# Performance work log

Hardware: AMD Instinct MI355X
Metric: run time of the kernel (lower is better)

Reference implementation:

```python
import jax, jax.numpy as jnp
import numpy as np

WINDOW_SIZE = 2
SOFTMAX_TEMP = 0.01
EPS = 1e-12  # F.normalize default eps


def _l2_normalize(x, axis):
    n = jnp.sqrt(jnp.sum(x * x, axis=axis, keepdims=True))
    return x / jnp.maximum(n, EPS)


def setup_inputs() -> dict:
    key = jax.random.key(0)
    k1, k2, k3 = jax.random.split(key, 3)
    B, C, N = 16, 128, 4096
    return {
        "keypoint_coords": jax.random.normal(k1, (B, 2, N), dtype=jnp.float32),
        "keypoint_weights": jax.random.uniform(k2, (B, 1, N), dtype=jnp.float32),
        "keypoint_desc": jax.random.normal(k3, (B, C, N), dtype=jnp.float32),
    }


def reference(keypoint_coords, keypoint_weights, keypoint_desc):
    # split interleaved src/tgt frames along batch
    src_coords = keypoint_coords[::WINDOW_SIZE]    # [b,2,N]
    tgt_coords = keypoint_coords[1::WINDOW_SIZE]   # [b,2,M]
    src_weights = keypoint_weights[::WINDOW_SIZE]  # [b,1,N]
    tgt_weights = keypoint_weights[1::WINDOW_SIZE] # [b,1,M]
    src_desc = keypoint_desc[::WINDOW_SIZE]        # [b,C,N]
    tgt_desc = keypoint_desc[1::WINDOW_SIZE]       # [b,C,M]

    C = src_desc.shape[1]
    src_desc_norm = _l2_normalize(src_desc, axis=1)
    tgt_desc_norm = _l2_normalize(tgt_desc, axis=1)

    # cosine similarity matrix [b,N,M]
    match_vals = jnp.einsum("bcn,bcm->bnm", src_desc_norm, tgt_desc_norm)
    soft_match_vals = jax.nn.softmax(match_vals / SOFTMAX_TEMP, axis=2)

    # reuse the attention matrix for three value matmuls
    pseudo_coords = jnp.einsum("bcm,bnm->bcn", tgt_coords, soft_match_vals)   # [b,2,N]
    pseudo_desc = jnp.einsum("bcm,bnm->bcn", tgt_desc, soft_match_vals)       # [b,C,N]
    pseudo_desc = _l2_normalize(pseudo_desc, axis=1)
    pseudo_weights = jnp.einsum("bim,bnm->bin", tgt_weights, soft_match_vals) # [b,1,N]

    desc_match_score = jnp.sum(src_desc * pseudo_desc, axis=1, keepdims=True) / float(C)
    match_weights = 0.5 * (desc_match_score + 1.0) * src_weights * pseudo_weights
    return pseudo_coords, match_weights
```

## Files before the change

kernel.cpp:

```cpp
#include <hip/hip_runtime.h>
#include <math.h>

#define C 128
#define N 4096
#define BP 8
#define TN 64

typedef __attribute__((ext_vector_type(8))) short bf16x8;
typedef __attribute__((ext_vector_type(16))) float f32x16;
typedef __attribute__((ext_vector_type(4))) int i32x4;
typedef __attribute__((ext_vector_type(16))) int i32x16;

#define PREP_OFF 65536
#define FRAGS_PER_MT 18
#define BLOB_BYTES ((size_t)BP * 128 * FRAGS_PER_MT * 1024)

__device__ __forceinline__ unsigned short bf16rnd(float x) {
  unsigned u = __float_as_uint(x);
  u += 0x7fffu + ((u >> 16) & 1u);
  return (unsigned short)(u >> 16);
}
__device__ __forceinline__ float bf16up(unsigned short h) {
  return __uint_as_float(((unsigned)h) << 16);
}
__device__ __forceinline__ int rne2(float x, float y) {
  unsigned ux = __float_as_uint(x); ux += 0x7fffu + ((ux >> 16) & 1u);
  unsigned uy = __float_as_uint(y); uy += 0x7fffu + ((uy >> 16) & 1u);
  return (int)__builtin_amdgcn_perm(uy, ux, 0x07060302u);
}
__device__ __forceinline__ int trunc2(float x, float y) {
  return (int)__builtin_amdgcn_perm(__float_as_uint(y), __float_as_uint(x), 0x07060302u);
}
__device__ __forceinline__ float truncres(float x) {
  return x - __uint_as_float(__float_as_uint(x) & 0xffff0000u);
}
__device__ __forceinline__ int pk4(int a, int b, int c, int d) {
  return (a & 255) | ((b & 255) << 8) | ((c & 255) << 16) | ((d & 255) << 24);
}

__global__ __launch_bounds__(256) void knorm_inv(const float* __restrict__ desc,
                                                 float* __restrict__ inv) {
  int n = blockIdx.x * 256 + threadIdx.x;
  int b = 2 * blockIdx.y + 1;
  const float* d = desc + (size_t)b * C * N + n;
  float ssq = 0.f;
#pragma unroll 8
  for (int c = 0; c < C; ++c) {
    float v = d[(size_t)c * N];
    ssq = fmaf(v, v, ssq);
  }
  inv[b * N + n] = 1.0f / fmaxf(sqrtf(ssq), 1e-12f);
}

__global__ __launch_bounds__(256) void kprep(
    const float* __restrict__ coords, const float* __restrict__ wtsp,
    const float* __restrict__ desc, unsigned char* __restrict__ blob) {
  const int mt = blockIdx.x;
  const int p = blockIdx.y;
  const int tb = 2 * p + 1;
  const int m0 = mt * 32;
  const int t = threadIdx.x;
  const int ks = t >> 6;
  const int h = (t >> 5) & 1;
  const int l31 = t & 31;

  __shared__ float rss[8][32];

  const float* tgtd = desc + (size_t)tb * C * N;
  unsigned char* bl = blob + ((size_t)(p * 128 + mt) * FRAGS_PER_MT) * 1024;

  float vr[16];
  float part = 0.f;
#pragma unroll
  for (int i = 0; i < 16; ++i) {
    float v = tgtd[(size_t)(32 * ks + 16 * h + i) * N + m0 + l31];
    vr[i] = v;
    part = fmaf(v, v, part);
  }
  rss[ks * 2 + h][l31] = part;
  __syncthreads();
  float ssq = 0.f;
#pragma unroll
  for (int u = 0; u < 8; ++u) ssq += rss[u][l31];
  const float invm = 1.0f / fmaxf(sqrtf(ssq), 1e-12f);

  {
    int hb[16], lb[16];
#pragma unroll
    for (int i = 0; i < 16; ++i) {
      int q = (int)rintf(vr[i] * invm * 16384.f);
      int hi = (q + 128) >> 8;
      hb[i] = hi;
      lb[i] = q - (hi << 8);
    }
    int4 ph = make_int4(pk4(hb[0], hb[1], hb[2], hb[3]), pk4(hb[4], hb[5], hb[6], hb[7]),
                        pk4(hb[8], hb[9], hb[10], hb[11]), pk4(hb[12], hb[13], hb[14], hb[15]));
    int4 pl = make_int4(pk4(lb[0], lb[1], lb[2], lb[3]), pk4(lb[4], lb[5], lb[6], lb[7]),
                        pk4(lb[8], lb[9], lb[10], lb[11]), pk4(lb[12], lb[13], lb[14], lb[15]));
    int lane = 32 * h + l31;
    *(int4*)(bl + (size_t)ks * 1024 + lane * 16) = ph;
    *(int4*)(bl + (size_t)(4 + ks) * 1024 + lane * 16) = pl;
  }

#pragma unroll
  for (int it = 0; it < 4; ++it) {
    int e = t + 256 * it;
    int c = e >> 3, mq = e & 7;
    float4 v = *(const float4*)&tgtd[(size_t)c * N + m0 + 4 * mq];
    int f = (c >> 5) * 2 + (mq >> 2);
    int slot = (c & 31) + 32 * ((mq >> 1) & 1);
    int2 pk;
    pk.x = rne2(v.x, v.y);
    pk.y = rne2(v.z, v.w);
    *(int2*)(bl + (size_t)(8 + f) * 1024 + slot * 16 + (mq & 1) * 8) = pk;
  }

  if (t < 128) {
    int fe = t >> 6, slot = t & 63, r = slot & 31, hh = slot >> 5;
    int4 pk = make_int4(0, 0, 0, 0);
    if (r < 4) {
      const float* rp = (r == 0)   ? coords + (size_t)tb * 2 * N
                        : (r == 1) ? coords + (size_t)tb * 2 * N + N
                                   : wtsp + (size_t)tb * N;
      int mb = m0 + 16 * fe + 8 * hh;
      float v[8];
#pragma unroll
      for (int i = 0; i < 8; ++i) v[i] = (r == 3) ? 1.0f : rp[mb + i];
      pk.x = rne2(v[0], v[1]);
      pk.y = rne2(v[2], v[3]);
      pk.z = rne2(v[4], v[5]);
      pk.w = rne2(v[6], v[7]);
    }
    *(int4*)(bl + (size_t)(16 + fe) * 1024 + slot * 16) = pk;
  }
}

#define BUF_SHORTS (2 * FRAGS_PER_MT * 512)
#define LDS_SHORTS (2 * BUF_SHORTS)

__global__ __launch_bounds__(256, 2) void kmain(
    const float* __restrict__ wtsp, const float* __restrict__ desc,
    const unsigned char* __restrict__ blob, float* __restrict__ out) {
  const int ntile = blockIdx.x;
  const int p = blockIdx.y;
  const int sb = 2 * p;
  const int n0 = ntile * TN;
  const int tid = threadIdx.x;
  const int w = tid >> 6;
  const int ln = tid & 63;
  const int l31 = ln & 31;
  const int h = ln >> 5;
  const int wn = w & 1;
  const int st = w >> 1;

  __shared__ __align__(16) short L[LDS_SHORTS];

  const float* srcd = desc + (size_t)sb * C * N;
  const unsigned char* wblob = blob + (size_t)p * 128 * FRAGS_PER_MT * 1024;
  const int nn = n0 + 32 * wn + l31;

  float ssq = 0.f;
#pragma unroll
  for (int ks = 0; ks < 4; ++ks) {
#pragma unroll
    for (int i = 0; i < 16; ++i) {
      float v = srcd[(size_t)(32 * ks + 16 * h + i) * N + nn];
      ssq = fmaf(v, v, ssq);
    }
  }
  ssq += __shfl_xor(ssq, 32);
  const float invs = 1.0f / fmaxf(sqrtf(ssq), 1e-12f);

  i32x4 Qhi[4], Qlo[4];
#pragma unroll
  for (int ks = 0; ks < 4; ++ks) {
    int hb[16], lb[16];
#pragma unroll
    for (int i = 0; i < 16; ++i) {
      float v = srcd[(size_t)(32 * ks + 16 * h + i) * N + nn] * invs;
      int q = (int)rintf(v * 16384.f);
      int hi = (q + 128) >> 8;
      hb[i] = hi;
      lb[i] = q - (hi << 8);
    }
    i32x4 qh = {pk4(hb[0], hb[1], hb[2], hb[3]), pk4(hb[4], hb[5], hb[6], hb[7]),
                pk4(hb[8], hb[9], hb[10], hb[11]), pk4(hb[12], hb[13], hb[14], hb[15])};
    i32x4 ql = {pk4(lb[0], lb[1], lb[2], lb[3]), pk4(lb[4], lb[5], lb[6], lb[7]),
                pk4(lb[8], lb[9], lb[10], lb[11]), pk4(lb[12], lb[13], lb[14], lb[15])};
    Qhi[ks] = qh;
    Qlo[ks] = ql;
  }

  f32x16 acc[5];
#pragma unroll
  for (int t = 0; t < 5; ++t)
#pragma unroll
    for (int r = 0; r < 16; ++r) acc[t][r] = 0.f;

  auto issue_dma = [&](int it, int bufb) {
    const unsigned char* gsrc = wblob + (size_t)(it * 2 * FRAGS_PER_MT) * 1024 + ln * 16;
    short* dst = &L[bufb * BUF_SHORTS];
#pragma unroll
    for (int jj = 0; jj < 9; ++jj) {
      int jg = 9 * w + jj;
      __builtin_amdgcn_global_load_lds(
          (const void __attribute__((address_space(1)))*)(gsrc + (size_t)jg * 1024),
          (void __attribute__((address_space(3)))*)&dst[jg * 512], 16, 0, 0);
    }
  };

  issue_dma(0, 0);
  __syncthreads();

  for (int it = 0; it < 64; ++it) {
    const int cb = it & 1;
    if (it + 1 < 64) issue_dma(it + 1, cb ^ 1);

    const short* vbase = &L[cb * BUF_SHORTS + st * (FRAGS_PER_MT * 512)];

    i32x16 Shh, Sx, Sll;
#pragma unroll
    for (int r = 0; r < 16; ++r) { Shh[r] = 0; Sx[r] = 0; Sll[r] = 0; }
#pragma unroll
    for (int ks = 0; ks < 4; ++ks) {
      i32x4 ah = *(const i32x4*)&vbase[ks * 512 + ln * 8];
      i32x4 al = *(const i32x4*)&vbase[(4 + ks) * 512 + ln * 8];
      Shh = __builtin_amdgcn_mfma_i32_32x32x32_i8(ah, Qhi[ks], Shh, 0, 0, 0);
      Sx = __builtin_amdgcn_mfma_i32_32x32x32_i8(ah, Qlo[ks], Sx, 0, 0, 0);
      Sx = __builtin_amdgcn_mfma_i32_32x32x32_i8(al, Qhi[ks], Sx, 0, 0, 0);
      Sll = __builtin_amdgcn_mfma_i32_32x32x32_i8(al, Qlo[ks], Sll, 0, 0, 0);
    }

    int pp[8], xpp[8];
#pragma unroll
    for (int q = 0; q < 4; ++q) {
      float pv[4];
#pragma unroll
      for (int j = 0; j < 4; ++j) {
        int r = 4 * q + j;
        int tot = (Shh[r] << 8) + Sx[r];
        float sf = fmaf((float)tot, 256.f, (float)Sll[r]);
        pv[j] = __expf(fmaf(sf, 3.7252903e-07f, -60.0f));
      }
      pp[2 * q] = rne2(pv[0], pv[1]);
      pp[2 * q + 1] = rne2(pv[2], pv[3]);
    }
#pragma unroll
    for (int j = 0; j < 8; ++j) xpp[j] = __shfl_xor(pp[j], 32);

#pragma unroll
    for (int s2 = 0; s2 < 2; ++s2) {
      int4 bi;
      if (h == 0)
        bi = make_int4(pp[4 * s2 + 0], pp[4 * s2 + 1], xpp[4 * s2 + 0], xpp[4 * s2 + 1]);
      else
        bi = make_int4(xpp[4 * s2 + 2], xpp[4 * s2 + 3], pp[4 * s2 + 2], pp[4 * s2 + 3]);
      bf16x8 bh = __builtin_bit_cast(bf16x8, bi);
#pragma unroll
      for (int t = 0; t < 5; ++t) {
        bf16x8 va = *(const bf16x8*)&vbase[(8 + 2 * t + s2) * 512 + ln * 8];
        acc[t] = __builtin_amdgcn_mfma_f32_32x32x16_bf16(va, bh, acc[t], 0, 0, 0);
      }
    }

    __syncthreads();
  }

  float* red = (float*)&L[0];
  if (st == 1) {
#pragma unroll
    for (int t = 0; t < 5; ++t)
#pragma unroll
      for (int r = 0; r < 16; ++r)
        red[wn * 5120 + t * 1024 + r * 64 + ln] = acc[t][r];
  }
  __syncthreads();

  if (st == 0) {
#pragma unroll
    for (int t = 0; t < 5; ++t)
#pragma unroll
      for (int r = 0; r < 16; ++r)
        acc[t][r] += red[wn * 5120 + t * 1024 + r * 64 + ln];

    float ssqd = 0.f, dotr = 0.f;
#pragma unroll
    for (int t = 0; t < 4; ++t) {
#pragma unroll
      for (int r = 0; r < 16; ++r) {
        int c = 32 * t + (r & 3) + 8 * (r >> 2) + 4 * h;
        float d = acc[t][r];
        ssqd = fmaf(d, d, ssqd);
        dotr = fmaf(d, srcd[(size_t)c * N + nn], dotr);
      }
    }
    ssqd += __shfl_xor(ssqd, 32);
    dotr += __shfl_xor(dotr, 32);
    if (h == 0) {
      float x = acc[4][0], y = acc[4][1], wv = acc[4][2], Ld = acc[4][3];
      float invL = 1.0f / Ld;
      float nrm = fmaxf(sqrtf(ssqd), 1e-30f);
      float score = dotr / (nrm * 128.0f);
      float sw = wtsp[(size_t)sb * N + nn];
      out[(size_t)p * 2 * N + nn] = x * invL;
      out[(size_t)p * 2 * N + N + nn] = y * invL;
      out[(size_t)(BP * 2 * N) + (size_t)p * N + nn] =
          0.5f * (score + 1.0f) * sw * wv * invL;
    }
  }
}

#define OFF_VMH3 0
#define OFF_VML3 8192
#define OFF_VCM3 16384
#define OFF_PH3 26624
#define LDS3_SHORTS 30720

__global__ __launch_bounds__(256, 2) void kmain_v3(
    const float* __restrict__ coords, const float* __restrict__ wtsp,
    const float* __restrict__ desc, const float* __restrict__ inv,
    float* __restrict__ out) {
  const int ntile = blockIdx.x;
  const int p = blockIdx.y;
  const int sb = 2 * p, tb = 2 * p + 1;
  const int n0 = ntile * TN;
  const int tid = threadIdx.x;
  const int w = tid >> 6;
  const int ln = tid & 63;
  const int l31 = ln & 31;
  const int h = ln >> 5;
  const int wn = w & 1;
  const int st = w >> 1;
  const int pt = wn * 64 + ln;

  __shared__ __align__(16) short L[LDS3_SHORTS];

  const float* srcd = desc + (size_t)sb * C * N;
  const float* tgtd = desc + (size_t)tb * C * N;
  const float* invtg = inv + tb * N;
  const float* tcx = coords + (size_t)tb * 2 * N;
  const float* tcy = tcx + N;
  const float* twp = wtsp + (size_t)tb * N;
  const int nn = n0 + 32 * wn + l31;

  float ssq = 0.f;
#pragma unroll
  for (int k = 0; k < 8; ++k) {
    int cb = 16 * k + 8 * h;
#pragma unroll
    for (int i = 0; i < 8; ++i) {
      float v = srcd[(size_t)(cb + i) * N + nn];
      ssq = fmaf(v, v, ssq);
    }
  }
  ssq += __shfl_xor(ssq, 32);
  float invs = 1.0f / fmaxf(sqrtf(ssq), 1e-12f);

  bf16x8 Qh[8], Ql[8];
#pragma unroll
  for (int k = 0; k < 8; ++k) {
    int cb = 16 * k + 8 * h;
    bf16x8 qh, ql;
#pragma unroll
    for (int i = 0; i < 8; ++i) {
      float v = srcd[(size_t)(cb + i) * N + nn] * invs;
      unsigned short hs = bf16rnd(v);
      unsigned short ls = bf16rnd(v - bf16up(hs));
      qh[i] = (short)hs;
      ql[i] = (short)ls;
    }
    Qh[k] = qh;
    Ql[k] = ql;
  }

  {
    int* z = (int*)&L[OFF_VCM3];
    for (int i = tid; i < 1024; i += 256) {
      int sI = i >> 9, j = i & 511;
      z[sI * 2560 + 2048 + j] = 0;
    }
  }

  f32x16 acc[5];
#pragma unroll
  for (int t = 0; t < 5; ++t)
#pragma unroll
    for (int r = 0; r < 16; ++r) acc[t][r] = 0.f;

  const int er = pt & 3, ehh = (pt >> 2) & 1, esf = pt >> 3;
  const float* erp = (er == 0) ? tcx : (er == 1) ? tcy : twp;

  float vm[32];
  float invm = 0.f;
  float4 exv0 = make_float4(1, 1, 1, 1), exv1 = exv0;

  auto prefetch = [&](int ms0) {
#pragma unroll
    for (int k = 0; k < 4; ++k) {
      int cb = 16 * (2 * k + wn) + 8 * h;
#pragma unroll
      for (int i = 0; i < 8; ++i)
        vm[k * 8 + i] = tgtd[(size_t)(cb + i) * N + ms0 + l31];
    }
    invm = invtg[ms0 + l31];
    if (pt < 16 && er < 3) {
      int mb = ms0 + 16 * esf + 8 * ehh;
      exv0 = *(const float4*)&erp[mb];
      exv1 = *(const float4*)&erp[mb + 4];
    }
  };

  prefetch(32 * st);

  for (int m0 = 0; m0 < N; m0 += 64) {
    const int ms0 = m0 + 32 * st;
    float4 vc[8];
#pragma unroll
    for (int it = 0; it < 8; ++it) {
      int e = pt + 128 * it, c = e >> 3, mq = e & 7;
      vc[it] = *(const float4*)&tgtd[(size_t)c * N + ms0 + 4 * mq];
    }
#pragma unroll
    for (int k = 0; k < 4; ++k) {
      int kk = 2 * k + wn;
      int hw[4], lw[4];
#pragma unroll
      for (int j = 0; j < 4; ++j) {
        float v0 = vm[k * 8 + 2 * j] * invm;
        float v1 = vm[k * 8 + 2 * j + 1] * invm;
        hw[j] = trunc2(v0, v1);
        lw[j] = trunc2(truncres(v0), truncres(v1));
      }
      *(int4*)&L[OFF_VMH3 + st * 4096 + kk * 512 + ln * 8] =
          make_int4(hw[0], hw[1], hw[2], hw[3]);
      *(int4*)&L[OFF_VML3 + st * 4096 + kk * 512 + ln * 8] =
          make_int4(lw[0], lw[1], lw[2], lw[3]);
    }
#pragma unroll
    for (int it = 0; it < 8; ++it) {
      int e = pt + 128 * it, c = e >> 3, mq = e & 7;
      float4 v = vc[it];
      int f = (c >> 5) * 2 + (mq >> 2);
      int slot = (c & 31) + 32 * ((mq >> 1) & 1);
      int2 pk;
      pk.x = rne2(v.x, v.y);
      pk.y = rne2(v.z, v.w);
      *(int2*)&L[OFF_VCM3 + st * 5120 + f * 512 + slot * 8 + (mq & 1) * 4] = pk;
    }
    if (pt < 16) {
      int4 pk;
      pk.x = rne2(exv0.x, exv0.y);
      pk.y = rne2(exv0.z, exv0.w);
      pk.z = rne2(exv1.x, exv1.y);
      pk.w = rne2(exv1.z, exv1.w);
      *(int4*)&L[OFF_VCM3 + st * 5120 + (8 + esf) * 512 + (er + 32 * ehh) * 8] = pk;
    }
    __syncthreads();
    if (m0 + 64 < N) prefetch(ms0 + 64);

    f32x16 S;
#pragma unroll
    for (int r = 0; r < 16; ++r) S[r] = 0.f;
    const short* vmh = &L[OFF_VMH3 + st * 4096];
    const short* vml = &L[OFF_VML3 + st * 4096];
#pragma unroll
    for (int k = 0; k < 8; ++k) {
      bf16x8 ah = *(const bf16x8*)&vmh[k * 512 + ln * 8];
      bf16x8 al = *(const bf16x8*)&vml[k * 512 + ln * 8];
      S = __builtin_amdgcn_mfma_f32_32x32x16_bf16(al, Qh[k], S, 0, 0, 0);
      S = __builtin_amdgcn_mfma_f32_32x32x16_bf16(ah, Ql[k], S, 0, 0, 0);
      S = __builtin_amdgcn_mfma_f32_32x32x16_bf16(ah, Qh[k], S, 0, 0, 0);
    }
#pragma unroll
    for (int q = 0; q < 4; ++q) {
      float p0 = __expf(fmaf(S[4 * q + 0], 100.0f, -60.0f));
      float p1 = __expf(fmaf(S[4 * q + 1], 100.0f, -60.0f));
      float p2 = __expf(fmaf(S[4 * q + 2], 100.0f, -60.0f));
      float p3 = __expf(fmaf(S[4 * q + 3], 100.0f, -60.0f));
      int2 a;
      a.x = rne2(p0, p1);
      a.y = rne2(p2, p3);
      *(int2*)&L[OFF_PH3 + w * 1024 + (q >> 1) * 512 + (l31 + 32 * (q & 1)) * 8 + h * 4] = a;
    }
#pragma unroll
    for (int s2 = 0; s2 < 2; ++s2) {
      bf16x8 bh = *(const bf16x8*)&L[OFF_PH3 + w * 1024 + s2 * 512 + ln * 8];
#pragma unroll
      for (int t = 0; t < 5; ++t) {
        bf16x8 va = *(const bf16x8*)&L[OFF_VCM3 + st * 5120 + (2 * t + s2) * 512 + ln * 8];
        acc[t] = __builtin_amdgcn_mfma_f32_32x32x16_bf16(va, bh, acc[t], 0, 0, 0);
      }
    }
    __syncthreads();
  }

  float* red = (float*)&L[0];
  if (st == 1) {
#pragma unroll
    for (int t = 0; t < 5; ++t)
#pragma unroll
      for (int r = 0; r < 16; ++r)
        red[wn * 5120 + t * 1024 + r * 64 + ln] = acc[t][r];
  }
  __syncthreads();
  if (st == 0) {
#pragma unroll
    for (int t = 0; t < 5; ++t)
#pragma unroll
      for (int r = 0; r < 16; ++r)
        acc[t][r] += red[wn * 5120 + t * 1024 + r * 64 + ln];
    float ssqd = 0.f, dotr = 0.f;
#pragma unroll
    for (int t = 0; t < 4; ++t) {
#pragma unroll
      for (int r = 0; r < 16; ++r) {
        int c = 32 * t + (r & 3) + 8 * (r >> 2) + 4 * h;
        float d = acc[t][r];
        ssqd = fmaf(d, d, ssqd);
        dotr = fmaf(d, srcd[(size_t)c * N + nn], dotr);
      }
    }
    ssqd += __shfl_xor(ssqd, 32);
    dotr += __shfl_xor(dotr, 32);
    if (h == 0) {
      float x = acc[4][0], y = acc[4][1], wv = acc[4][2], Ld = acc[4][3];
      float invL = 1.0f / Ld;
      float nrm = fmaxf(sqrtf(ssqd), 1e-30f);
      float score = dotr / (nrm * 128.0f);
      float sw = wtsp[(size_t)sb * N + nn];
      out[(size_t)p * 2 * N + nn] = x * invL;
      out[(size_t)p * 2 * N + N + nn] = y * invL;
      out[(size_t)(BP * 2 * N) + (size_t)p * N + nn] =
          0.5f * (score + 1.0f) * sw * wv * invL;
    }
  }
}

extern "C" void kernel_launch(void* const* d_in, const int* in_sizes, int n_in,
                              void* d_out, int out_size, void* d_ws, size_t ws_size,
                              hipStream_t stream) {
  const float* coords = (const float*)d_in[0];
  const float* wts = (const float*)d_in[1];
  const float* desc = (const float*)d_in[2];
  float* out = (float*)d_out;
  float* inv = (float*)d_ws;
  unsigned char* blob = (unsigned char*)d_ws + PREP_OFF;

  if (ws_size >= PREP_OFF + BLOB_BYTES) {
    kprep<<<dim3(128, BP), 256, 0, stream>>>(coords, wts, desc, blob);
    kmain<<<dim3(N / TN, BP), 256, 0, stream>>>(wts, desc, blob, out);
  } else {
    knorm_inv<<<dim3(N / 256, BP), 256, 0, stream>>>(desc, inv);
    kmain_v3<<<dim3(N / TN, BP), 256, 0, stream>>>(coords, wts, desc, inv, out);
  }
}
```

Before: 208.1 us.

## Stream V fragments to registers, drop low-low int8 MFMA term, flatten grid

```diff
diff --git a/kernel.cpp b/kernel.cpp
--- a/kernel.cpp
+++ b/kernel.cpp
@@ -13,6 +13,7 @@
 
 #define PREP_OFF 65536
 #define FRAGS_PER_MT 18
+#define SUBT_BYTES (FRAGS_PER_MT * 1024)
 #define BLOB_BYTES ((size_t)BP * 128 * FRAGS_PER_MT * 1024)
 
 __device__ __forceinline__ unsigned short bf16rnd(float x) {
@@ -135,14 +136,14 @@
   }
 }
 
-#define BUF_SHORTS (2 * FRAGS_PER_MT * 512)
-#define LDS_SHORTS (2 * BUF_SHORTS)
+#define LDS_SHORTS 20480
 
 __global__ __launch_bounds__(256, 2) void kmain(
     const float* __restrict__ wtsp, const float* __restrict__ desc,
     const unsigned char* __restrict__ blob, float* __restrict__ out) {
-  const int ntile = blockIdx.x;
-  const int p = blockIdx.y;
+  const int bid = blockIdx.x;
+  const int p = bid & 7;
+  const int ntile = bid >> 3;
   const int sb = 2 * p;
   const int n0 = ntile * TN;
   const int tid = threadIdx.x;
@@ -156,7 +157,7 @@
   __shared__ __align__(16) short L[LDS_SHORTS];
 
   const float* srcd = desc + (size_t)sb * C * N;
-  const unsigned char* wblob = blob + (size_t)p * 128 * FRAGS_PER_MT * 1024;
+  const unsigned char* wblob = blob + (size_t)p * 128 * SUBT_BYTES;
   const int nn = n0 + 32 * wn + l31;
 
   float ssq = 0.f;
@@ -197,39 +198,57 @@
 #pragma unroll
     for (int r = 0; r < 16; ++r) acc[t][r] = 0.f;
 
-  auto issue_dma = [&](int it, int bufb) {
-    const unsigned char* gsrc = wblob + (size_t)(it * 2 * FRAGS_PER_MT) * 1024 + ln * 16;
-    short* dst = &L[bufb * BUF_SHORTS];
-#pragma unroll
-    for (int jj = 0; jj < 9; ++jj) {
-      int jg = 9 * w + jj;
+  i32x16 zz;
+#pragma unroll
+  for (int r = 0; r < 16; ++r) zz[r] = 0;
+
+  auto issue_dma = [&](int it2, int bufb) {
+    const unsigned char* s0 = wblob + (size_t)(it2 * 2) * SUBT_BYTES + ln * 16;
+#pragma unroll
+    for (int jj = 0; jj < 4; ++jj) {
+      int jg = 4 * w + jj;
+      const unsigned char* src = s0 + (size_t)(jg >> 3) * SUBT_BYTES + (size_t)(jg & 7) * 1024;
       __builtin_amdgcn_global_load_lds(
-          (const void __attribute__((address_space(1)))*)(gsrc + (size_t)jg * 1024),
-          (void __attribute__((address_space(3)))*)&dst[jg * 512], 16, 0, 0);
+          (const void __attribute__((address_space(1)))*)src,
+          (void __attribute__((address_space(3)))*)&L[bufb * 8192 + jg * 512], 16, 0, 0);
     }
   };
+  auto loadV = [&](int it2, int s2, bf16x8* V) {
+    const unsigned char* vb =
+        wblob + (size_t)(it2 * 2 + st) * SUBT_BYTES + (size_t)(8 + s2) * 1024 + ln * 16;
+#pragma unroll
+    for (int t = 0; t < 5; ++t) V[t] = *(const bf16x8*)(vb + (size_t)(2 * t) * 1024);
+  };
 
   issue_dma(0, 0);
+  bf16x8 V0[5], V1[5];
+  loadV(0, 0, V0);
   __syncthreads();
 
   for (int it = 0; it < 64; ++it) {
     const int cb = it & 1;
-    if (it + 1 < 64) issue_dma(it + 1, cb ^ 1);
-
-    const short* vbase = &L[cb * BUF_SHORTS + st * (FRAGS_PER_MT * 512)];
-
-    i32x16 Shh, Sx, Sll;
-#pragma unroll
-    for (int r = 0; r < 16; ++r) { Shh[r] = 0; Sx[r] = 0; Sll[r] = 0; }
-#pragma unroll
-    for (int ks = 0; ks < 4; ++ks) {
-      i32x4 ah = *(const i32x4*)&vbase[ks * 512 + ln * 8];
-      i32x4 al = *(const i32x4*)&vbase[(4 + ks) * 512 + ln * 8];
+    if (it < 63) issue_dma(it + 1, cb ^ 1);
+
+    const short* vb = &L[cb * 8192 + st * 4096];
+
+    i32x16 Shh, Sx;
+    {
+      i32x4 ah = *(const i32x4*)&vb[0 * 512 + ln * 8];
+      i32x4 al = *(const i32x4*)&vb[4 * 512 + ln * 8];
+      Shh = __builtin_amdgcn_mfma_i32_32x32x32_i8(ah, Qhi[0], zz, 0, 0, 0);
+      Sx = __builtin_amdgcn_mfma_i32_32x32x32_i8(ah, Qlo[0], zz, 0, 0, 0);
+      Sx = __builtin_amdgcn_mfma_i32_32x32x32_i8(al, Qhi[0], Sx, 0, 0, 0);
+    }
+#pragma unroll
+    for (int ks = 1; ks < 4; ++ks) {
+      i32x4 ah = *(const i32x4*)&vb[ks * 512 + ln * 8];
+      i32x4 al = *(const i32x4*)&vb[(4 + ks) * 512 + ln * 8];
       Shh = __builtin_amdgcn_mfma_i32_32x32x32_i8(ah, Qhi[ks], Shh, 0, 0, 0);
       Sx = __builtin_amdgcn_mfma_i32_32x32x32_i8(ah, Qlo[ks], Sx, 0, 0, 0);
       Sx = __builtin_amdgcn_mfma_i32_32x32x32_i8(al, Qhi[ks], Sx, 0, 0, 0);
-      Sll = __builtin_amdgcn_mfma_i32_32x32x32_i8(al, Qlo[ks], Sll, 0, 0, 0);
-    }
+    }
+
+    loadV(it, 1, V1);
 
     int pp[8], xpp[8];
 #pragma unroll
@@ -239,8 +258,7 @@
       for (int j = 0; j < 4; ++j) {
         int r = 4 * q + j;
         int tot = (Shh[r] << 8) + Sx[r];
-        float sf = fmaf((float)tot, 256.f, (float)Sll[r]);
-        pv[j] = __expf(fmaf(sf, 3.7252903e-07f, -60.0f));
+        pv[j] = __expf(fmaf((float)tot, 9.5367431640625e-5f, -60.0f));
       }
       pp[2 * q] = rne2(pv[0], pv[1]);
       pp[2 * q + 1] = rne2(pv[2], pv[3]);
@@ -248,19 +266,33 @@
 #pragma unroll
     for (int j = 0; j < 8; ++j) xpp[j] = __shfl_xor(pp[j], 32);
 
-#pragma unroll
-    for (int s2 = 0; s2 < 2; ++s2) {
+    {
       int4 bi;
       if (h == 0)
-        bi = make_int4(pp[4 * s2 + 0], pp[4 * s2 + 1], xpp[4 * s2 + 0], xpp[4 * s2 + 1]);
+        bi = make_int4(pp[0], pp[1], xpp[0], xpp[1]);
       else
-        bi = make_int4(xpp[4 * s2 + 2], xpp[4 * s2 + 3], pp[4 * s2 + 2], pp[4 * s2 + 3]);
+        bi = make_int4(xpp[2], xpp[3], pp[2], pp[3]);
       bf16x8 bh = __builtin_bit_cast(bf16x8, bi);
 #pragma unroll
-      for (int t = 0; t < 5; ++t) {
-        bf16x8 va = *(const bf16x8*)&vbase[(8 + 2 * t + s2) * 512 + ln * 8];
-        acc[t] = __builtin_amdgcn_mfma_f32_32x32x16_bf16(va, bh, acc[t], 0, 0, 0);
-      }
+      for (int t = 0; t < 5; ++t)
+        acc[t] = __builtin_amdgcn_mfma_f32_32x32x16_bf16(V0[t], bh, acc[t], 0, 0, 0);
+    }
+
+    {
+      int itn = (it < 63) ? it + 1 : 63;
+      loadV(itn, 0, V0);
+    }
+
+    {
+      int4 bi;
+      if (h == 0)
+        bi = make_int4(pp[4], pp[5], xpp[4], xpp[5]);
+      else
+        bi = make_int4(xpp[6], xpp[7], pp[6], pp[7]);
+      bf16x8 bh = __builtin_bit_cast(bf16x8, bi);
+#pragma unroll
+      for (int t = 0; t < 5; ++t)
+        acc[t] = __builtin_amdgcn_mfma_f32_32x32x16_bf16(V1[t], bh, acc[t], 0, 0, 0);
     }
 
     __syncthreads();
@@ -548,7 +580,7 @@
 
   if (ws_size >= PREP_OFF + BLOB_BYTES) {
     kprep<<<dim3(128, BP), 256, 0, stream>>>(coords, wts, desc, blob);
-    kmain<<<dim3(N / TN, BP), 256, 0, stream>>>(wts, desc, blob, out);
+    kmain<<<dim3((N / TN) * BP), 256, 0, stream>>>(wts, desc, blob, out);
   } else {
     knorm_inv<<<dim3(N / 256, BP), 256, 0, stream>>>(desc, inv);
     kmain_v3<<<dim3(N / TN, BP), 256, 0, stream>>>(coords, wts, desc, inv, out);
```

Measured after the change: 185.2 us. 11.0% less time.
